# Optimization experiments

Hardware: AMD Instinct MI355X
Metric: run time of the kernel (lower is better)

Reference implementation:

```python
import jax, jax.numpy as jnp
import numpy as np

T, B, E, H = 256, 8, 512, 32
EXP = 512            # number of expanded (periodic-image) keys
SMOOTH = 20.0        # smooth_factor


def setup_inputs() -> dict:
    key = jax.random.key(0)
    ks = jax.random.split(key, 12)
    s = 1.0 / np.sqrt(E)
    return {
        "query": jax.random.normal(ks[0], (T, B, E), dtype=jnp.float32),
        "outcell_index": jax.random.randint(ks[1], (B, EXP), 0, T),
        "expand_mask": jax.random.bernoulli(ks[2], 0.1, (B, EXP)),
        "key_padding_mask": jax.random.bernoulli(ks[3], 0.1, (B, T)),
        "local_attention_weight": jax.random.uniform(ks[4], (B, T, T + EXP), dtype=jnp.float32),
        "Wq": jax.random.normal(ks[5], (E, E), dtype=jnp.float32) * s,
        "bq": jnp.zeros((E,), dtype=jnp.float32),
        "Wk": jax.random.normal(ks[6], (E, E), dtype=jnp.float32) * s,   # k_bias=False
        "Wv": jax.random.normal(ks[7], (E, E), dtype=jnp.float32) * s,
        "bv": jnp.zeros((E,), dtype=jnp.float32),
        "Wo": jax.random.normal(ks[8], (E, E), dtype=jnp.float32) * s,
        "bo": jnp.zeros((E,), dtype=jnp.float32),
    }


def reference(query, outcell_index, expand_mask, key_padding_mask,
              local_attention_weight, Wq, bq, Wk, Wv, bv, Wo, bo):
    t, b, e = query.shape
    hd = e // H
    # QKV projections (torch Linear: y = x @ W.T + b)
    q = jnp.einsum('tbe,fe->tbf', query, Wq) + bq
    k = jnp.einsum('tbe,fe->tbf', query, Wk)          # no k bias
    v = jnp.einsum('tbe,fe->tbf', query, Wv) + bv
    # PBC gather-expand K/V along the time axis
    oc = outcell_index.T[:, :, None]                  # [EXP, B, 1]
    k = jnp.concatenate([k, jnp.take_along_axis(k, oc, axis=0)], axis=0)  # [S,B,E]
    v = jnp.concatenate([v, jnp.take_along_axis(v, oc, axis=0)], axis=0)
    s_len = k.shape[0]
    # [len, B, E] -> [B, H, len, hd]
    qh = q.reshape(t, b, H, hd).transpose(1, 2, 0, 3)
    kh = k.reshape(s_len, b, H, hd).transpose(1, 2, 0, 3)
    vh = v.reshape(s_len, b, H, hd).transpose(1, 2, 0, 3)
    # NOTE: forward() never applies self.scaling in this path (faithful)
    scores = jnp.einsum('bhtd,bhsd->bhts', qh, kh)    # [B,H,T,S]
    law = local_attention_weight[:, None]             # [B,1,T,S]
    scores = (scores + SMOOTH) * law - SMOOTH         # smooth softmax
    kpm = jnp.concatenate([key_padding_mask, expand_mask], axis=1)  # [B,S]
    scores = jnp.where(kpm[:, None, None, :], -jnp.inf, scores)
    probs = jax.nn.softmax(scores, axis=-1)
    probs = probs * law                               # post-softmax reweight
    attn = jnp.einsum('bhts,bhsd->bhtd', probs, vh)   # [B,H,T,hd]
    attn = attn.transpose(2, 0, 1, 3).reshape(t, b, e)
    return jnp.einsum('tbe,fe->tbf', attn, Wo) + bo
```

## Files before the change

### kernel.cpp

```cpp
#include <hip/hip_runtime.h>
#include <stdint.h>

#define T_ 256
#define B_ 8
#define E_ 512
#define H_ 32
#define HD_ 16
#define EXP_ 512
#define S_ 768
#define M_ 2048
#define SMOOTH_ 20.0f
#define PSTR 36
#define VSTR 800

typedef __attribute__((ext_vector_type(8)))  short bf16x8;
typedef __attribute__((ext_vector_type(4)))  float f32x4;
typedef __attribute__((ext_vector_type(16))) float f32x16;

__device__ __forceinline__ unsigned int pk2(float a, float b)
{
    unsigned int ua = __float_as_uint(a);
    ua = ua + 0x7FFFu + ((ua >> 16) & 1u);
    unsigned int ub = __float_as_uint(b);
    ub = ub + 0x7FFFu + ((ub >> 16) & 1u);
    return (ua >> 16) | (ub & 0xFFFF0000u);
}
__device__ __forceinline__ ushort bf1(float a)
{
    unsigned int u = __float_as_uint(a);
    u = u + 0x7FFFu + ((u >> 16) & 1u);
    return (ushort)(u >> 16);
}

union U16 { uint4 u; bf16x8 v; };

__global__ __launch_bounds__(256)
void conv_kernel(const float* __restrict__ X,
                 const float* __restrict__ Wq, const float* __restrict__ Wk,
                 const float* __restrict__ Wv, const float* __restrict__ Wo,
                 ushort* __restrict__ Xb, ushort* __restrict__ Wb)
{
    const int seg = blockIdx.x >> 6;
    const int blk = blockIdx.x & 63;
    const float* src;
    ushort* dst;
    if (seg < 4) { src = X + (size_t)seg * 262144; dst = Xb + (size_t)seg * 262144; }
    else {
        const float* ws_[4] = {Wq, Wk, Wv, Wo};
        src = ws_[seg - 4];
        dst = Wb + (size_t)(seg - 4) * 262144;
    }
    const int base = blk * 4096 + threadIdx.x * 16;
    float4 f0 = *(const float4*)&src[base + 0];
    float4 f1 = *(const float4*)&src[base + 4];
    float4 f2 = *(const float4*)&src[base + 8];
    float4 f3 = *(const float4*)&src[base + 12];
    *(uint4*)&dst[base + 0] = make_uint4(pk2(f0.x, f0.y), pk2(f0.z, f0.w),
                                         pk2(f1.x, f1.y), pk2(f1.z, f1.w));
    *(uint4*)&dst[base + 8] = make_uint4(pk2(f2.x, f2.y), pk2(f2.z, f2.w),
                                         pk2(f3.x, f3.y), pk2(f3.z, f3.w));
}

__device__ __forceinline__ void mfma_gemm_body_bf(const ushort* __restrict__ X,
                                                  const ushort* __restrict__ W,
                                                  int m0, int n0,
                                                  f32x4 acc[2][2],
                                                  ushort* As, ushort* Bs)
{
    const int tid  = threadIdx.x;
    const int lrow = tid >> 2;
    const int kq   = tid & 3;
    const int l    = tid & 63;
    const int w    = tid >> 6;
    const int wm   = w & 1;
    const int wn   = w >> 1;
    const int lq   = l >> 4;
    const int ln   = l & 15;

    const ushort* Xr = &X[(size_t)(m0 + lrow) * E_ + kq * 16];
    const ushort* Wr = &W[(size_t)(n0 + lrow) * E_ + kq * 16];
    ushort* Aw = &As[lrow * 72 + kq * 16];
    ushort* Bw = &Bs[lrow * 72 + kq * 16];

    for (int k0 = 0; k0 < E_; k0 += 64) {
        uint4 a0 = *(const uint4*)&Xr[k0 + 0];
        uint4 a1 = *(const uint4*)&Xr[k0 + 8];
        uint4 b0 = *(const uint4*)&Wr[k0 + 0];
        uint4 b1 = *(const uint4*)&Wr[k0 + 8];
        __syncthreads();
        *(uint4*)&Aw[0] = a0;
        *(uint4*)&Aw[8] = a1;
        *(uint4*)&Bw[0] = b0;
        *(uint4*)&Bw[8] = b1;
        __syncthreads();
#pragma unroll
        for (int kb = 0; kb < 2; ++kb) {
            bf16x8 af0 = *(const bf16x8*)&As[(32 * wm + ln) * 72 + 32 * kb + lq * 8];
            bf16x8 af1 = *(const bf16x8*)&As[(32 * wm + 16 + ln) * 72 + 32 * kb + lq * 8];
            bf16x8 bf0 = *(const bf16x8*)&Bs[(32 * wn + ln) * 72 + 32 * kb + lq * 8];
            bf16x8 bf1 = *(const bf16x8*)&Bs[(32 * wn + 16 + ln) * 72 + 32 * kb + lq * 8];
            acc[0][0] = __builtin_amdgcn_mfma_f32_16x16x32_bf16(af0, bf0, acc[0][0], 0, 0, 0);
            acc[0][1] = __builtin_amdgcn_mfma_f32_16x16x32_bf16(af0, bf1, acc[0][1], 0, 0, 0);
            acc[1][0] = __builtin_amdgcn_mfma_f32_16x16x32_bf16(af1, bf0, acc[1][0], 0, 0, 0);
            acc[1][1] = __builtin_amdgcn_mfma_f32_16x16x32_bf16(af1, bf1, acc[1][1], 0, 0, 0);
        }
    }
}

__global__ __launch_bounds__(256)
void qkv_gemm(const ushort* __restrict__ Xb, const ushort* __restrict__ Wb,
              const float* __restrict__ bq, const float* __restrict__ bv,
              ushort* __restrict__ Qb, ushort* __restrict__ Kb,
              ushort* __restrict__ VTb)
{
    __shared__ __align__(16) ushort As[64 * 72];
    __shared__ __align__(16) ushort Bs[64 * 72];
    const int z = blockIdx.z;
    const ushort* W    = Wb + (size_t)z * 262144;
    const float*  bias = (z == 0) ? bq : (z == 2 ? bv : nullptr);

    const int m0 = blockIdx.y * 64;
    const int n0 = blockIdx.x * 64;

    f32x4 acc[2][2];
#pragma unroll
    for (int i = 0; i < 2; ++i)
#pragma unroll
        for (int j = 0; j < 2; ++j)
            acc[i][j] = (f32x4){0.f, 0.f, 0.f, 0.f};

    mfma_gemm_body_bf(Xb, W, m0, n0, acc, As, Bs);

    const int l  = threadIdx.x & 63;
    const int w  = threadIdx.x >> 6;
    const int wm = w & 1;
    const int wn = w >> 1;
    const int lq = l >> 4;
    const int ln = l & 15;

#pragma unroll
    for (int j = 0; j < 2; ++j) {
        const int nb = n0 + 32 * wn + 16 * j;
        const int h  = nb >> 4;
        const int d  = ln;
        const float bv_ = bias ? bias[nb + ln] : 0.f;
#pragma unroll
        for (int i = 0; i < 2; ++i) {
#pragma unroll
            for (int r = 0; r < 4; ++r) {
                const int m = m0 + 32 * wm + 16 * i + lq * 4 + r;
                const int t = m >> 3;
                const int b = m & 7;
                const int bh = b * H_ + h;
                const ushort val = bf1(acc[i][j][r] + bv_);
                if (z == 0)      Qb[((size_t)bh * T_ + t) * HD_ + d] = val;
                else if (z == 1) Kb[((size_t)bh * T_ + t) * HD_ + d] = val;
                else             VTb[((size_t)bh * HD_ + d) * T_ + t] = val;
            }
        }
    }
}

__global__ __launch_bounds__(256)
void out_gemm(const ushort* __restrict__ Ab, const ushort* __restrict__ Wob,
              const float* __restrict__ bo, float* __restrict__ dst)
{
    __shared__ __align__(16) ushort As[64 * 72];
    __shared__ __align__(16) ushort Bs[64 * 72];
    const int m0 = blockIdx.y * 64;
    const int n0 = blockIdx.x * 64;

    f32x4 acc[2][2];
#pragma unroll
    for (int i = 0; i < 2; ++i)
#pragma unroll
        for (int j = 0; j < 2; ++j)
            acc[i][j] = (f32x4){0.f, 0.f, 0.f, 0.f};

    mfma_gemm_body_bf(Ab, Wob, m0, n0, acc, As, Bs);

    const int l  = threadIdx.x & 63;
    const int w  = threadIdx.x >> 6;
    const int wm = w & 1;
    const int wn = w >> 1;
    const int lq = l >> 4;
    const int ln = l & 15;

#pragma unroll
    for (int j = 0; j < 2; ++j) {
        const int nb = n0 + 32 * wn + 16 * j;
        const float bo_ = bo[nb + ln];
#pragma unroll
        for (int i = 0; i < 2; ++i) {
#pragma unroll
            for (int r = 0; r < 4; ++r) {
                const int m = m0 + 32 * wm + 16 * i + lq * 4 + r;
                dst[(size_t)m * E_ + nb + ln] = acc[i][j][r] + bo_;
            }
        }
    }
}

__global__ __launch_bounds__(256)
void attn_kernel(const ushort* __restrict__ Qb, const ushort* __restrict__ Kb,
                 const ushort* __restrict__ VTb, const float* __restrict__ LAW,
                 const int* __restrict__ kpm, const int* __restrict__ em,
                 const int* __restrict__ oc, ushort* __restrict__ Ab)
{
    __shared__ __align__(16) ushort Ks[S_ * HD_];
    __shared__ __align__(16) ushort Vt[HD_ * VSTR];
    __shared__ __align__(16) float  msf[S_];
    __shared__ __align__(16) float  Zbuf[128];
    __shared__ __align__(16) ushort Pb[4][32 * PSTR];

    const int tid    = threadIdx.x;
    const int blk    = blockIdx.x;
    const int bh     = blk >> 1;
    const int thalf  = blk & 1;
    const int b      = bh >> 5;
    const int h      = bh & 31;

    {
        const uint4* src = (const uint4*)&Kb[(size_t)bh * T_ * HD_];
        uint4* dst = (uint4*)Ks;
        dst[tid]       = src[tid];
        dst[tid + 256] = src[tid + 256];
    }
    {
#pragma unroll
        for (int it = 0; it < 2; ++it) {
            const int f = tid + it * 256;
            const int row = f >> 5, ch = f & 31;
            *(uint4*)&Vt[row * VSTR + ch * 8] =
                *(const uint4*)&VTb[((size_t)bh * HD_ + row) * T_ + ch * 8];
        }
    }
    {
#pragma unroll
        for (int it = 0; it < 2; ++it) {
            const int j = tid + it * 256;
            const int src = oc[b * EXP_ + j];
            const uint4* kr = (const uint4*)&Kb[((size_t)bh * T_ + src) * HD_];
            *(uint4*)&Ks[(T_ + j) * HD_ + 0] = kr[0];
            *(uint4*)&Ks[(T_ + j) * HD_ + 8] = kr[1];
#pragma unroll
            for (int d = 0; d < 16; ++d)
                Vt[d * VSTR + T_ + j] = VTb[((size_t)bh * HD_ + d) * T_ + src];
        }
    }
    {
#pragma unroll
        for (int it = 0; it < 3; ++it) {
            const int s = tid + it * 256;
            const int m = (s < T_) ? kpm[b * T_ + s] : em[b * EXP_ + (s - T_)];
            msf[s] = m ? 0.f : 1.f;
        }
    }

    const int w      = tid >> 6;
    const int l      = tid & 63;
    const int tloc   = l & 31;
    const int khalf  = l >> 5;
    const int tglob  = thalf * 128 + w * 32 + tloc;
    bf16x8 qf = *(const bf16x8*)&Qb[((size_t)bh * T_ + tglob) * HD_ + khalf * 8];

    __syncthreads();

    const f32x16 zero16 = {0.f,0.f,0.f,0.f,0.f,0.f,0.f,0.f,
                           0.f,0.f,0.f,0.f,0.f,0.f,0.f,0.f};
    f32x4 o0 = {0.f, 0.f, 0.f, 0.f};
    f32x4 o1 = {0.f, 0.f, 0.f, 0.f};
    float Z = 0.f;

    const float* lawp = &LAW[((size_t)b * T_ + tglob) * S_];
    ushort* prow = &Pb[w][tloc * PSTR];
    const int tl = l & 15;
    const int kg = l >> 4;

    for (int i = 0; i < S_ / 32; ++i) {
        bf16x8 kf = *(const bf16x8*)&Ks[(i * 32 + tloc) * HD_ + khalf * 8];
        f32x16 sc = __builtin_amdgcn_mfma_f32_32x32x16_bf16(kf, qf, zero16, 0, 0, 0);

#pragma unroll
        for (int qd = 0; qd < 4; ++qd) {
            const int sb = i * 32 + qd * 8 + khalf * 4;
            float4 mf = *(const float4*)&msf[sb];
            float4 lw = *(const float4*)&lawp[sb];
            float e0, e1, e2, e3;
            {
                float x = (sc[qd*4+0] + SMOOTH_) * lw.x - SMOOTH_;
                e0 = mf.x * __expf(x - 50.f);
                x = (sc[qd*4+1] + SMOOTH_) * lw.y - SMOOTH_;
                e1 = mf.y * __expf(x - 50.f);
                x = (sc[qd*4+2] + SMOOTH_) * lw.z - SMOOTH_;
                e2 = mf.z * __expf(x - 50.f);
                x = (sc[qd*4+3] + SMOOTH_) * lw.w - SMOOTH_;
                e3 = mf.w * __expf(x - 50.f);
            }
            Z += (e0 + e1) + (e2 + e3);
            *(uint2*)&prow[qd * 8 + khalf * 4] =
                make_uint2(pk2(e0 * lw.x, e1 * lw.y), pk2(e2 * lw.z, e3 * lw.w));
        }

        bf16x8 vf = *(const bf16x8*)&Vt[tl * VSTR + i * 32 + kg * 8];
        {
            const ushort* pr0 = &Pb[w][(0 * 16 + tl) * PSTR + kg * 8];
            U16 u;
            uint2 a0 = *(const uint2*)pr0;
            uint2 a1 = *(const uint2*)(pr0 + 4);
            u.u = make_uint4(a0.x, a0.y, a1.x, a1.y);
            o0 = __builtin_amdgcn_mfma_f32_16x16x32_bf16(vf, u.v, o0, 0, 0, 0);
            const ushort* pr1 = &Pb[w][(1 * 16 + tl) * PSTR + kg * 8];
            uint2 b0 = *(const uint2*)pr1;
            uint2 b1 = *(const uint2*)(pr1 + 4);
            u.u = make_uint4(b0.x, b0.y, b1.x, b1.y);
            o1 = __builtin_amdgcn_mfma_f32_16x16x32_bf16(vf, u.v, o1, 0, 0, 0);
        }
    }

    Z += __shfl_xor(Z, 32);
    if (l < 32) Zbuf[w * 32 + tloc] = Z;
    __syncthreads();

#pragma unroll
    for (int th = 0; th < 2; ++th) {
        const float Zt  = Zbuf[w * 32 + th * 16 + tl];
        const float inv = (Zt > 0.f) ? 1.f / Zt : 0.f;
        const int   t   = thalf * 128 + w * 32 + th * 16 + tl;
        const f32x4 o   = th ? o1 : o0;
#pragma unroll
        for (int r = 0; r < 4; ++r) {
            const int d = kg * 4 + r;
            Ab[((size_t)t * B_ + b) * E_ + h * HD_ + d] = bf1(o[r] * inv);
        }
    }
}

extern "C" void kernel_launch(void* const* d_in, const int* in_sizes, int n_in,
                              void* d_out, int out_size, void* d_ws, size_t ws_size,
                              hipStream_t stream)
{
    const float* query = (const float*)d_in[0];
    const int*   oc    = (const int*)d_in[1];
    const int*   em    = (const int*)d_in[2];
    const int*   kpm   = (const int*)d_in[3];
    const float* law   = (const float*)d_in[4];
    const float* Wq    = (const float*)d_in[5];
    const float* bq    = (const float*)d_in[6];
    const float* Wk    = (const float*)d_in[7];
    const float* Wv    = (const float*)d_in[8];
    const float* bv    = (const float*)d_in[9];
    const float* Wo    = (const float*)d_in[10];
    const float* bo    = (const float*)d_in[11];
    float* out = (float*)d_out;

    ushort* Xb  = (ushort*)d_ws;
    ushort* Wb  = Xb  + (size_t)1048576;
    ushort* Qb  = Wb  + (size_t)1048576;
    ushort* Kb  = Qb  + (size_t)1048576;
    ushort* VTb = Kb  + (size_t)1048576;
    ushort* Ab  = VTb + (size_t)1048576;

    conv_kernel<<<512, 256, 0, stream>>>(query, Wq, Wk, Wv, Wo, Xb, Wb);

    dim3 gq(E_ / 64, M_ / 64, 3);
    qkv_gemm<<<gq, 256, 0, stream>>>(Xb, Wb, bq, bv, Qb, Kb, VTb);

    attn_kernel<<<B_ * H_ * 2, 256, 0, stream>>>(Qb, Kb, VTb, law, kpm, em, oc, Ab);

    dim3 go(E_ / 64, M_ / 64, 1);
    out_gemm<<<go, 256, 0, stream>>>(Ab, Wb + (size_t)3 * 262144, bo, out);
}
```

Measured before the change: 130.1 us.

## Split attention key range across two wave groups with LDS reduction

Doubles the attention block to 512 threads. Each query tile is now handled by two waves, each covering half of the 768 keys, and the partial outputs and normalizers are merged through LDS that reuses the K buffer. The goal is more wave-level parallelism and latency hiding on the serial key loop, which also streams the large LAW array. The cost is an extra barrier and a cross-wave reduction, plus higher per-block resource use that may reduce how many blocks fit per CU.

```diff
diff --git a/kernel.cpp b/kernel.cpp
--- a/kernel.cpp
+++ b/kernel.cpp
@@ -12,6 +12,7 @@
 #define SMOOTH_ 20.0f
 #define PSTR 36
 #define VSTR 800
+#define OSTR 20
 
 typedef __attribute__((ext_vector_type(8)))  short bf16x8;
 typedef __attribute__((ext_vector_type(4)))  float f32x4;
@@ -201,7 +202,7 @@
     }
 }
 
-__global__ __launch_bounds__(256)
+__global__ __launch_bounds__(512)
 void attn_kernel(const ushort* __restrict__ Qb, const ushort* __restrict__ Kb,
                  const ushort* __restrict__ VTb, const float* __restrict__ LAW,
                  const int* __restrict__ kpm, const int* __restrict__ em,
@@ -210,8 +211,10 @@
     __shared__ __align__(16) ushort Ks[S_ * HD_];
     __shared__ __align__(16) ushort Vt[HD_ * VSTR];
     __shared__ __align__(16) float  msf[S_];
-    __shared__ __align__(16) float  Zbuf[128];
-    __shared__ __align__(16) ushort Pb[4][32 * PSTR];
+    __shared__ __align__(16) ushort Pb[8][32 * PSTR];
+
+    float* Obuf = (float*)Ks;
+    float* Zb   = (float*)Ks + 128 * OSTR;
 
     const int tid    = threadIdx.x;
     const int blk    = blockIdx.x;
@@ -220,40 +223,29 @@
     const int b      = bh >> 5;
     const int h      = bh & 31;
 
+    ((uint4*)Ks)[tid] = ((const uint4*)&Kb[(size_t)bh * T_ * HD_])[tid];
     {
-        const uint4* src = (const uint4*)&Kb[(size_t)bh * T_ * HD_];
-        uint4* dst = (uint4*)Ks;
-        dst[tid]       = src[tid];
-        dst[tid + 256] = src[tid + 256];
+        const int row = tid >> 5, ch = tid & 31;
+        *(uint4*)&Vt[row * VSTR + ch * 8] =
+            *(const uint4*)&VTb[((size_t)bh * HD_ + row) * T_ + ch * 8];
     }
     {
-#pragma unroll
-        for (int it = 0; it < 2; ++it) {
-            const int f = tid + it * 256;
-            const int row = f >> 5, ch = f & 31;
-            *(uint4*)&Vt[row * VSTR + ch * 8] =
-                *(const uint4*)&VTb[((size_t)bh * HD_ + row) * T_ + ch * 8];
-        }
+        const int j   = tid;
+        const int src = oc[b * EXP_ + j];
+        const uint4* kr = (const uint4*)&Kb[((size_t)bh * T_ + src) * HD_];
+        *(uint4*)&Ks[(T_ + j) * HD_ + 0] = kr[0];
+        *(uint4*)&Ks[(T_ + j) * HD_ + 8] = kr[1];
+#pragma unroll
+        for (int d = 0; d < 16; ++d)
+            Vt[d * VSTR + T_ + j] = VTb[((size_t)bh * HD_ + d) * T_ + src];
     }
     {
-#pragma unroll
-        for (int it = 0; it < 2; ++it) {
-            const int j = tid + it * 256;
-            const int src = oc[b * EXP_ + j];
-            const uint4* kr = (const uint4*)&Kb[((size_t)bh * T_ + src) * HD_];
-            *(uint4*)&Ks[(T_ + j) * HD_ + 0] = kr[0];
-            *(uint4*)&Ks[(T_ + j) * HD_ + 8] = kr[1];
-#pragma unroll
-            for (int d = 0; d < 16; ++d)
-                Vt[d * VSTR + T_ + j] = VTb[((size_t)bh * HD_ + d) * T_ + src];
-        }
-    }
-    {
-#pragma unroll
-        for (int it = 0; it < 3; ++it) {
-            const int s = tid + it * 256;
-            const int m = (s < T_) ? kpm[b * T_ + s] : em[b * EXP_ + (s - T_)];
-            msf[s] = m ? 0.f : 1.f;
+        const int s = tid;
+        const int m = (s < T_) ? kpm[b * T_ + s] : em[b * EXP_ + (s - T_)];
+        msf[s] = m ? 0.f : 1.f;
+        if (tid < 256) {
+            const int s2 = 512 + tid;
+            msf[s2] = em[b * EXP_ + (s2 - T_)] ? 0.f : 1.f;
         }
     }
 
@@ -261,7 +253,9 @@
     const int l      = tid & 63;
     const int tloc   = l & 31;
     const int khalf  = l >> 5;
-    const int tglob  = thalf * 128 + w * 32 + tloc;
+    const int wt     = w & 3;
+    const int sh     = w >> 2;
+    const int tglob  = thalf * 128 + wt * 32 + tloc;
     bf16x8 qf = *(const bf16x8*)&Qb[((size_t)bh * T_ + tglob) * HD_ + khalf * 8];
 
     __syncthreads();
@@ -277,7 +271,7 @@
     const int tl = l & 15;
     const int kg = l >> 4;
 
-    for (int i = 0; i < S_ / 32; ++i) {
+    for (int i = sh * 12; i < sh * 12 + 12; ++i) {
         bf16x8 kf = *(const bf16x8*)&Ks[(i * 32 + tloc) * HD_ + khalf * 8];
         f32x16 sc = __builtin_amdgcn_mfma_f32_32x32x16_bf16(kf, qf, zero16, 0, 0, 0);
 
@@ -319,19 +313,35 @@
     }
 
     Z += __shfl_xor(Z, 32);
-    if (l < 32) Zbuf[w * 32 + tloc] = Z;
+
     __syncthreads();
 
-#pragma unroll
-    for (int th = 0; th < 2; ++th) {
-        const float Zt  = Zbuf[w * 32 + th * 16 + tl];
-        const float inv = (Zt > 0.f) ? 1.f / Zt : 0.f;
-        const int   t   = thalf * 128 + w * 32 + th * 16 + tl;
-        const f32x4 o   = th ? o1 : o0;
-#pragma unroll
-        for (int r = 0; r < 4; ++r) {
-            const int d = kg * 4 + r;
-            Ab[((size_t)t * B_ + b) * E_ + h * HD_ + d] = bf1(o[r] * inv);
+    if (sh == 1) {
+#pragma unroll
+        for (int th = 0; th < 2; ++th) {
+            const f32x4 o = th ? o1 : o0;
+            *(float4*)&Obuf[((wt * 2 + th) * 16 + tl) * OSTR + kg * 4] =
+                make_float4(o[0], o[1], o[2], o[3]);
+        }
+        if (l < 32) Zb[wt * 32 + tloc] = Z;
+    }
+    __syncthreads();
+
+    if (sh == 0) {
+        const float Ztot = Z + Zb[wt * 32 + tloc];
+#pragma unroll
+        for (int th = 0; th < 2; ++th) {
+            const float Zt  = __shfl(Ztot, th * 16 + tl);
+            const float inv = (Zt > 0.f) ? 1.f / Zt : 0.f;
+            float4 po = *(const float4*)&Obuf[((wt * 2 + th) * 16 + tl) * OSTR + kg * 4];
+            const f32x4 o = th ? o1 : o0;
+            const int t = thalf * 128 + wt * 32 + th * 16 + tl;
+            float ov[4] = {o[0] + po.x, o[1] + po.y, o[2] + po.z, o[3] + po.w};
+#pragma unroll
+            for (int r = 0; r < 4; ++r) {
+                const int d = kg * 4 + r;
+                Ab[((size_t)t * B_ + b) * E_ + h * HD_ + d] = bf1(ov[r] * inv);
+            }
         }
     }
 }
@@ -366,7 +376,7 @@
     dim3 gq(E_ / 64, M_ / 64, 3);
     qkv_gemm<<<gq, 256, 0, stream>>>(Xb, Wb, bq, bv, Qb, Kb, VTb);
 
-    attn_kernel<<<B_ * H_ * 2, 256, 0, stream>>>(Qb, Kb, VTb, law, kpm, em, oc, Ab);
+    attn_kernel<<<B_ * H_ * 2, 512, 0, stream>>>(Qb, Kb, VTb, law, kpm, em, oc, Ab);
 
     dim3 go(E_ / 64, M_ / 64, 1);
     out_gemm<<<go, 256, 0, stream>>>(Ab, Wb + (size_t)3 * 262144, bo, out);
```

Result: no change. 130.5 us (+0.3%).
